# Optimization experiments

Hardware: AMD Instinct MI355X
Metric: run time of the kernel (lower is better)

The kernel has to match this reference:

```python
import jax, jax.numpy as jnp
import numpy as np


def setup_inputs() -> dict:
    key = jax.random.key(0)
    ks_ = jax.random.split(key, 12)
    B, Q, K, D, d = 8, 4096, 4096, 256, 64
    s = 1.0 / np.sqrt(D)
    inp = {
        "qs": jax.random.normal(ks_[0], (B, Q, D), jnp.float32),
        "ks": jax.random.normal(ks_[1], (B, K, D), jnp.float32),
        "vs": jax.random.normal(ks_[2], (B, K, D), jnp.float32),
        "valid_lens": jax.random.randint(ks_[3], (B,), 1, K + 1, jnp.int32),
        "Wq": jax.random.normal(ks_[4], (D, d), jnp.float32) * s,
        "bq": jnp.zeros((d,), jnp.float32),
        "Wk": jax.random.normal(ks_[5], (D, d), jnp.float32) * s,
        "bk": jnp.zeros((d,), jnp.float32),
        "Wv": jax.random.normal(ks_[6], (D, d), jnp.float32) * s,
        "bv": jnp.zeros((d,), jnp.float32),
        "Wo": jax.random.normal(ks_[7], (d, d), jnp.float32) * (1.0 / np.sqrt(d)),
        "bo": jnp.zeros((d,), jnp.float32),
    }
    return inp


def reference(qs, ks, vs, valid_lens, Wq, bq, Wk, bk, Wv, bv, Wo, bo):
    # Linear projections (default MLP([64]) heads)
    q = qs @ Wq + bq          # [B, Q, d]
    k = ks @ Wk + bk          # [B, K, d]
    v = vs @ Wv + bv          # [B, K, d]

    # RBF kernel scores: exp(-||q_i - k_j||^2 / sqrt(d)).
    # Expand ||q-k||^2 = ||q||^2 + ||k||^2 - 2 q.k to avoid the [B,Q,K,d]
    # pairwise-difference tensor the original materializes.
    q2 = jnp.sum(q * q, axis=-1)                         # [B, Q]
    k2 = jnp.sum(k * k, axis=-1)                         # [B, K]
    qk = jnp.einsum("bqd,bkd->bqk", q, k)                # [B, Q, K]
    d_sq = jnp.maximum(q2[:, :, None] + k2[:, None, :] - 2.0 * qk, 0.0)
    attn = jnp.exp(-d_sq / jnp.sqrt(jnp.asarray(k.shape[-1], q.dtype)))

    # Mask invalid keys (fill=0.0), then row-normalize.
    key_ids = jnp.arange(k.shape[1])                     # [K]
    mask = key_ids[None, None, :] < valid_lens[:, None, None]
    attn = jnp.where(mask, attn, 0.0)
    attn = attn / jnp.sum(attn, axis=-1, keepdims=True)

    ctx = attn @ v                                       # [B, Q, d]
    out = ctx @ Wo + bo                                  # [B, Q, d]
    return out, attn
```

## Files before the change

### kernel.cpp

```cpp
#include <hip/hip_runtime.h>
#include <hip/hip_bf16.h>


typedef _Float16 HALF;
typedef HALF half8 __attribute__((ext_vector_type(8)));
typedef float f32x4 __attribute__((ext_vector_type(4)));

#define MFMA16(a, b, c) __builtin_amdgcn_mfma_f32_16x16x32_f16((a), (b), (c), 0, 0, 0)

union Cv4 { HALF h[4]; uint2 u; };
union Cv8 { HALF h[8]; uint4 u; };

__global__ __launch_bounds__(256) void k_prep(const float* __restrict__ Wq,
                                              const float* __restrict__ Wk,
                                              const float* __restrict__ Wv,
                                              const float* __restrict__ Wo,
                                              HALF* __restrict__ wt,
                                              HALF* __restrict__ wto) {
    int gid = blockIdx.x * 256 + threadIdx.x;
    if (gid < 49152) {
        int t = gid >> 14;
        int rem = gid & 16383;
        int n = rem >> 8, k = rem & 255;
        const float* W = (t == 0) ? Wq : ((t == 1) ? Wk : Wv);
        wt[gid] = (HALF)W[k * 64 + n];
    } else {
        int rem = gid - 49152;
        int n = rem >> 6, k = rem & 63;
        wto[rem] = (HALF)Wo[k * 64 + n];
    }
}

__global__ __launch_bounds__(256) void k_proj(const float* __restrict__ qs,
                                              const float* __restrict__ ks,
                                              const float* __restrict__ vs,
                                              const float* __restrict__ bq,
                                              const float* __restrict__ bk,
                                              const float* __restrict__ bv,
                                              const HALF* __restrict__ wt,
                                              HALF* __restrict__ qh,
                                              HALF* __restrict__ kh,
                                              HALF* __restrict__ vth,
                                              float* __restrict__ q2w,
                                              float* __restrict__ k2w) {
    int bid = blockIdx.x;
    int t = bid >> 9;
    int rem = bid & 511;
    int b = rem & 7, rt = rem >> 3;
    int m0 = rt * 64;
    const float* X    = (t == 0) ? qs : ((t == 1) ? ks : vs);
    const float* bias = (t == 0) ? bq : ((t == 1) ? bk : bv);

    __shared__ char smem[67584];
    HALF (*sW)[264]  = (HALF(*)[264])smem;
    HALF (*sX)[264]  = (HALF(*)[264])(smem + 33792);
    float (*sOut)[68] = (float(*)[68])(smem + 33792);

    int tid = threadIdx.x;
    int w = tid >> 6, lane = tid & 63, ln = lane & 15, quad = lane >> 4;

    const HALF* wsrc = wt + t * 16384;
#pragma unroll
    for (int s = 0; s < 8; ++s) {
        int flat = (s * 256 + tid) * 8;
        int r = flat >> 8, c = flat & 255;
        *(uint4*)&sW[r][c] = *(const uint4*)(wsrc + flat);
    }
    const float* xbase = X + ((size_t)(b * 4096 + m0)) * 256;
#pragma unroll
    for (int s = 0; s < 16; ++s) {
        int flat = (s * 256 + tid) * 4;
        int r = flat >> 8, c = flat & 255;
        float4 xv = *(const float4*)(xbase + flat);
        Cv4 cv; cv.h[0] = (HALF)xv.x; cv.h[1] = (HALF)xv.y;
        cv.h[2] = (HALF)xv.z; cv.h[3] = (HALF)xv.w;
        *(uint2*)&sX[r][c] = cv.u;
    }
    __syncthreads();

    f32x4 zero4 = {0.f, 0.f, 0.f, 0.f};
    f32x4 acc[4] = {zero4, zero4, zero4, zero4};
#pragma unroll
    for (int kb = 0; kb < 8; ++kb) {
        half8 a = *(half8*)&sX[w * 16 + ln][kb * 32 + quad * 8];
#pragma unroll
        for (int t4 = 0; t4 < 4; ++t4) {
            half8 bf = *(half8*)&sW[t4 * 16 + ln][kb * 32 + quad * 8];
            acc[t4] = MFMA16(a, bf, acc[t4]);
        }
    }
    __syncthreads();

    float bias_v[4];
#pragma unroll
    for (int t4 = 0; t4 < 4; ++t4) bias_v[t4] = bias[t4 * 16 + ln];

    float rsq[4] = {0.f, 0.f, 0.f, 0.f};
#pragma unroll
    for (int t4 = 0; t4 < 4; ++t4) {
#pragma unroll
        for (int r = 0; r < 4; ++r) {
            float v = acc[t4][r] + bias_v[t4];
            rsq[r] += v * v;
            sOut[w * 16 + quad * 4 + r][t4 * 16 + ln] = v;
        }
    }
    if (t < 2) {
        float* dst2 = (t == 0) ? q2w : k2w;
#pragma unroll
        for (int r = 0; r < 4; ++r) {
            float v = rsq[r];
#pragma unroll
            for (int off = 1; off < 16; off <<= 1) v += __shfl_xor(v, off);
            if (ln == 0) dst2[b * 4096 + m0 + w * 16 + quad * 4 + r] = v;
        }
    }
    __syncthreads();

    if (t < 2) {
        HALF* dst = ((t == 0) ? qh : kh) + ((size_t)(b * 4096 + m0)) * 64;
#pragma unroll
        for (int s = 0; s < 4; ++s) {
            int flat = (s * 256 + tid) * 4;
            int r = flat >> 6, c = flat & 63;
            float4 v = *(float4*)&sOut[r][c];
            Cv4 cv; cv.h[0] = (HALF)v.x; cv.h[1] = (HALF)v.y;
            cv.h[2] = (HALF)v.z; cv.h[3] = (HALF)v.w;
            *(uint2*)(dst + flat) = cv.u;
        }
    } else {
        HALF* dst = vth + (size_t)b * 64 * 4096 + m0;
#pragma unroll
        for (int s = 0; s < 2; ++s) {
            int dv = s * 32 + (tid >> 3);
            int kc = (tid & 7) * 8;
            Cv8 cv;
#pragma unroll
            for (int i = 0; i < 8; ++i) cv.h[i] = (HALF)sOut[kc + i][dv];
            *(uint4*)(dst + (size_t)dv * 4096 + kc) = cv.u;
        }
    }
}

__global__ __launch_bounds__(256) void k_attn(const HALF* __restrict__ qh,
                                              const HALF* __restrict__ kh,
                                              const HALF* __restrict__ vth,
                                              const float* __restrict__ q2w,
                                              const float* __restrict__ k2w,
                                              const int* __restrict__ vlen,
                                              float* __restrict__ attn_out,
                                              float* __restrict__ ctx_out) {
    int bid = blockIdx.x;
    int b = bid & 7, qt = bid >> 3;
    int m0 = qt * 64;
    int tid = threadIdx.x;
    int w = tid >> 6, lane = tid & 63, ln = lane & 15, quad = lane >> 4;
    int valid = vlen[b];

    __shared__ char smem[36608];
    HALF (*sK)[72]  = (HALF(*)[72])smem;
    HALF (*sVt)[72] = (HALF(*)[72])(smem + 9216);
    float (*sS)[68] = (float(*)[68])(smem + 18432);
    HALF (*sQ)[72]  = (HALF(*)[72])(smem + 18432);
    float* sQ2 = (float*)(smem + 35840);
    float* sK2 = sQ2 + 64;
    float* sRS = sK2 + 64;

    const HALF* qbase = qh + ((size_t)(b * 4096 + m0)) * 64;
#pragma unroll
    for (int s = 0; s < 2; ++s) {
        int flat = (s * 256 + tid) * 8;
        *(uint4*)&sQ[flat >> 6][flat & 63] = *(const uint4*)(qbase + flat);
    }
    if (tid < 64) sQ2[tid] = q2w[b * 4096 + m0 + tid];
    __syncthreads();

    half8 qa[2];
    {
        int row = w * 16 + ln, k0 = quad * 8;
        qa[0] = *(half8*)&sQ[row][k0];
        qa[1] = *(half8*)&sQ[row][32 + k0];
    }
    __syncthreads();

    int nvt = (valid + 63) >> 6;
    const HALF* kbb = kh + (size_t)b * 4096 * 64;
    const HALF* vtb = vth + (size_t)b * 64 * 4096;

    float rs[4] = {0.f, 0.f, 0.f, 0.f};

    for (int nt = 0; nt < nvt; ++nt) {
        int n0 = nt * 64;
#pragma unroll
        for (int s = 0; s < 2; ++s) {
            int flat = (s * 256 + tid) * 8;
            *(uint4*)&sK[flat >> 6][flat & 63] = *(const uint4*)(kbb + (size_t)n0 * 64 + flat);
        }
        if (tid < 64) sK2[tid] = k2w[b * 4096 + n0 + tid];
        __syncthreads();
#pragma unroll
        for (int t4 = 0; t4 < 4; ++t4) {
            f32x4 acc = {0.f, 0.f, 0.f, 0.f};
            half8 b0 = *(half8*)&sK[t4 * 16 + ln][quad * 8];
            half8 b1 = *(half8*)&sK[t4 * 16 + ln][32 + quad * 8];
            acc = MFMA16(qa[0], b0, acc);
            acc = MFMA16(qa[1], b1, acc);
            int col = t4 * 16 + ln;
            float k2v = sK2[col];
            bool ok = (n0 + col) < valid;
#pragma unroll
            for (int r = 0; r < 4; ++r) {
                int row = w * 16 + quad * 4 + r;
                float dsq = fmaxf(sQ2[row] + k2v - 2.f * acc[r], 0.f);
                float e = ok ? __expf(-0.125f * dsq) : 0.f;
                rs[r] += e;
            }
        }
        __syncthreads();
    }

#pragma unroll
    for (int r = 0; r < 4; ++r) {
        float v = rs[r];
#pragma unroll
        for (int off = 1; off < 16; off <<= 1) v += __shfl_xor(v, off);
        rs[r] = v;
    }
    if (ln == 0) {
#pragma unroll
        for (int r = 0; r < 4; ++r) sRS[w * 16 + quad * 4 + r] = rs[r];
    }
    __syncthreads();
    if (tid < 64) sRS[tid] = 1.0f / sRS[tid];
    __syncthreads();
    float inv_r[4];
#pragma unroll
    for (int r = 0; r < 4; ++r) inv_r[r] = sRS[w * 16 + quad * 4 + r];

    f32x4 cz = {0.f, 0.f, 0.f, 0.f};
    f32x4 cacc[4] = {cz, cz, cz, cz};
    float* attn_base = attn_out + ((size_t)(b * 4096 + m0)) * 4096;

    for (int nt = 0; nt < nvt; ++nt) {
        int n0 = nt * 64;
#pragma unroll
        for (int s = 0; s < 2; ++s) {
            int flat = (s * 256 + tid) * 8;
            *(uint4*)&sK[flat >> 6][flat & 63] = *(const uint4*)(kbb + (size_t)n0 * 64 + flat);
        }
#pragma unroll
        for (int s = 0; s < 2; ++s) {
            int flat = (s * 256 + tid) * 8;
            int dv = flat >> 6, c = flat & 63;
            *(uint4*)&sVt[dv][c] = *(const uint4*)(vtb + (size_t)dv * 4096 + n0 + c);
        }
        if (tid < 64) sK2[tid] = k2w[b * 4096 + n0 + tid];
        __syncthreads();
#pragma unroll
        for (int t4 = 0; t4 < 4; ++t4) {
            f32x4 acc = {0.f, 0.f, 0.f, 0.f};
            half8 b0 = *(half8*)&sK[t4 * 16 + ln][quad * 8];
            half8 b1 = *(half8*)&sK[t4 * 16 + ln][32 + quad * 8];
            acc = MFMA16(qa[0], b0, acc);
            acc = MFMA16(qa[1], b1, acc);
            int col = t4 * 16 + ln;
            float k2v = sK2[col];
            bool ok = (n0 + col) < valid;
#pragma unroll
            for (int r = 0; r < 4; ++r) {
                int row = w * 16 + quad * 4 + r;
                float dsq = fmaxf(sQ2[row] + k2v - 2.f * acc[r], 0.f);
                float e = ok ? __expf(-0.125f * dsq) : 0.f;
                sS[row][col] = e * inv_r[r];
            }
        }
        __syncthreads();
#pragma unroll
        for (int s = 0; s < 4; ++s) {
            int row = s * 16 + (tid >> 4);
            int col = (tid & 15) * 4;
            *(float4*)(attn_base + (size_t)row * 4096 + n0 + col) = *(float4*)&sS[row][col];
        }
#pragma unroll
        for (int ks2 = 0; ks2 < 2; ++ks2) {
            int row_a = w * 16 + ln;
            const float* sp = &sS[row_a][ks2 * 32 + quad * 8];
            float4 f0 = *(float4*)sp;
            float4 f1 = *((float4*)sp + 1);
            half8 pa = {(HALF)f0.x, (HALF)f0.y, (HALF)f0.z, (HALF)f0.w,
                        (HALF)f1.x, (HALF)f1.y, (HALF)f1.z, (HALF)f1.w};
#pragma unroll
            for (int t4 = 0; t4 < 4; ++t4) {
                half8 vb = *(half8*)&sVt[t4 * 16 + ln][ks2 * 32 + quad * 8];
                cacc[t4] = MFMA16(pa, vb, cacc[t4]);
            }
        }
        __syncthreads();
    }

    float4 z4 = {0.f, 0.f, 0.f, 0.f};
    for (int nt = nvt; nt < 64; ++nt) {
        int n0 = nt * 64;
#pragma unroll
        for (int s = 0; s < 4; ++s) {
            int row = s * 16 + (tid >> 4);
            int col = (tid & 15) * 4;
            *(float4*)(attn_base + (size_t)row * 4096 + n0 + col) = z4;
        }
    }

    float* ctx_base = ctx_out + ((size_t)(b * 4096 + m0)) * 64;
#pragma unroll
    for (int t4 = 0; t4 < 4; ++t4) {
#pragma unroll
        for (int r = 0; r < 4; ++r) {
            ctx_base[(size_t)(w * 16 + quad * 4 + r) * 64 + t4 * 16 + ln] = cacc[t4][r];
        }
    }
}

__global__ __launch_bounds__(256) void k_out(float* __restrict__ outg,
                                             const HALF* __restrict__ wto,
                                             const float* __restrict__ bo) {
    int bid = blockIdx.x;
    size_t row0 = (size_t)bid * 64;
    int tid = threadIdx.x;
    int w = tid >> 6, lane = tid & 63, ln = lane & 15, quad = lane >> 4;

    __shared__ char smem[18432];
    HALF (*sA)[72] = (HALF(*)[72])smem;
    HALF (*sB)[72] = (HALF(*)[72])(smem + 9216);

    float* gbase = outg + row0 * 64;
#pragma unroll
    for (int s = 0; s < 4; ++s) {
        int flat = (s * 256 + tid) * 4;
        int r = flat >> 6, c = flat & 63;
        float4 v = *(const float4*)(gbase + flat);
        Cv4 cv; cv.h[0] = (HALF)v.x; cv.h[1] = (HALF)v.y;
        cv.h[2] = (HALF)v.z; cv.h[3] = (HALF)v.w;
        *(uint2*)&sA[r][c] = cv.u;
    }
#pragma unroll
    for (int s = 0; s < 2; ++s) {
        int flat = (s * 256 + tid) * 8;
        *(uint4*)&sB[flat >> 6][flat & 63] = *(const uint4*)(wto + flat);
    }
    __syncthreads();

    f32x4 z = {0.f, 0.f, 0.f, 0.f};
    f32x4 acc[4] = {z, z, z, z};
#pragma unroll
    for (int ks2 = 0; ks2 < 2; ++ks2) {
        half8 a = *(half8*)&sA[w * 16 + ln][ks2 * 32 + quad * 8];
#pragma unroll
        for (int t4 = 0; t4 < 4; ++t4) {
            half8 bf = *(half8*)&sB[t4 * 16 + ln][ks2 * 32 + quad * 8];
            acc[t4] = MFMA16(a, bf, acc[t4]);
        }
    }
#pragma unroll
    for (int t4 = 0; t4 < 4; ++t4) {
        float bov = bo[t4 * 16 + ln];
#pragma unroll
        for (int r = 0; r < 4; ++r) {
            gbase[(size_t)(w * 16 + quad * 4 + r) * 64 + t4 * 16 + ln] = acc[t4][r] + bov;
        }
    }
}

extern "C" void kernel_launch(void* const* d_in, const int* in_sizes, int n_in,
                              void* d_out, int out_size, void* d_ws, size_t ws_size,
                              hipStream_t stream) {
    const float* qs = (const float*)d_in[0];
    const float* ks = (const float*)d_in[1];
    const float* vs = (const float*)d_in[2];
    const int* vlen = (const int*)d_in[3];
    const float* Wq = (const float*)d_in[4];
    const float* bq = (const float*)d_in[5];
    const float* Wk = (const float*)d_in[6];
    const float* bk = (const float*)d_in[7];
    const float* Wv = (const float*)d_in[8];
    const float* bv = (const float*)d_in[9];
    const float* Wo = (const float*)d_in[10];
    const float* bo = (const float*)d_in[11];

    float* out  = (float*)d_out;
    float* attn = out + 2097152;

    char* wsb = (char*)d_ws;
    HALF*  wt  = (HALF*)(wsb + 0);
    HALF*  wto = (HALF*)(wsb + 98304);
    HALF*  qh  = (HALF*)(wsb + 131072);
    HALF*  kh  = (HALF*)(wsb + 4325376);
    HALF*  vth = (HALF*)(wsb + 8519680);
    float* q2w = (float*)(wsb + 12713984);
    float* k2w = (float*)(wsb + 12845056);

    k_prep<<<208, 256, 0, stream>>>(Wq, Wk, Wv, Wo, wt, wto);
    k_proj<<<1536, 256, 0, stream>>>(qs, ks, vs, bq, bk, bv, wt, qh, kh, vth, q2w, k2w);
    k_attn<<<512, 256, 0, stream>>>(qh, kh, vth, q2w, k2w, vlen, attn, out);
    k_out<<<512, 256, 0, stream>>>(out, wto, bo);
}
```

Measured before the change: 793.0 us.

## Drop query norm term, prefetch K/V tiles, fuse output projection into attention

Computes attention scores as exp(q·k/4 - |k|^2/8), dropping the per-row |q|^2 factor that cancels in normalization and folding the key mask into a -inf per-key constant. K/V tiles are prefetched into registers for the next iteration while the current tile is computed. The output projection kernel is fused into the attention epilogue, which avoids the ctx round-trip through global memory. Batch-to-block mapping is skewed for load balance, and packed fp16 conversion is used. Removing |q|^2 changes numerical scaling, so exp values can be much larger than before and may risk overflow for large dot products.

```diff
diff --git a/kernel.cpp b/kernel.cpp
--- a/kernel.cpp
+++ b/kernel.cpp
@@ -4,12 +4,14 @@
 
 typedef _Float16 HALF;
 typedef HALF half8 __attribute__((ext_vector_type(8)));
+typedef __fp16 fp16x2 __attribute__((ext_vector_type(2)));
 typedef float f32x4 __attribute__((ext_vector_type(4)));
 
 #define MFMA16(a, b, c) __builtin_amdgcn_mfma_f32_16x16x32_f16((a), (b), (c), 0, 0, 0)
 
 union Cv4 { HALF h[4]; uint2 u; };
 union Cv8 { HALF h[8]; uint4 u; };
+union PK8 { fp16x2 p2[4]; half8 v; };
 
 __global__ __launch_bounds__(256) void k_prep(const float* __restrict__ Wq,
                                               const float* __restrict__ Wk,
@@ -31,18 +33,17 @@
     }
 }
 
-__global__ __launch_bounds__(256) void k_proj(const float* __restrict__ qs,
-                                              const float* __restrict__ ks,
-                                              const float* __restrict__ vs,
-                                              const float* __restrict__ bq,
-                                              const float* __restrict__ bk,
-                                              const float* __restrict__ bv,
-                                              const HALF* __restrict__ wt,
-                                              HALF* __restrict__ qh,
-                                              HALF* __restrict__ kh,
-                                              HALF* __restrict__ vth,
-                                              float* __restrict__ q2w,
-                                              float* __restrict__ k2w) {
+__global__ __launch_bounds__(256, 2) void k_proj(const float* __restrict__ qs,
+                                                 const float* __restrict__ ks,
+                                                 const float* __restrict__ vs,
+                                                 const float* __restrict__ bq,
+                                                 const float* __restrict__ bk,
+                                                 const float* __restrict__ bv,
+                                                 const HALF* __restrict__ wt,
+                                                 HALF* __restrict__ qh,
+                                                 HALF* __restrict__ kh,
+                                                 HALF* __restrict__ vth,
+                                                 float* __restrict__ kcw) {
     int bid = blockIdx.x;
     int t = bid >> 9;
     int rem = bid & 511;
@@ -105,14 +106,13 @@
             sOut[w * 16 + quad * 4 + r][t4 * 16 + ln] = v;
         }
     }
-    if (t < 2) {
-        float* dst2 = (t == 0) ? q2w : k2w;
+    if (t == 1) {
 #pragma unroll
         for (int r = 0; r < 4; ++r) {
             float v = rsq[r];
 #pragma unroll
             for (int off = 1; off < 16; off <<= 1) v += __shfl_xor(v, off);
-            if (ln == 0) dst2[b * 4096 + m0 + w * 16 + quad * 4 + r] = v;
+            if (ln == 0) kcw[b * 4096 + m0 + w * 16 + quad * 4 + r] = -0.125f * v;
         }
     }
     __syncthreads();
@@ -142,79 +142,77 @@
     }
 }
 
-__global__ __launch_bounds__(256) void k_attn(const HALF* __restrict__ qh,
-                                              const HALF* __restrict__ kh,
-                                              const HALF* __restrict__ vth,
-                                              const float* __restrict__ q2w,
-                                              const float* __restrict__ k2w,
-                                              const int* __restrict__ vlen,
-                                              float* __restrict__ attn_out,
-                                              float* __restrict__ ctx_out) {
+__global__ __launch_bounds__(256, 4) void k_attn(const HALF* __restrict__ qh,
+                                                 const HALF* __restrict__ kh,
+                                                 const HALF* __restrict__ vth,
+                                                 const float* __restrict__ kcw,
+                                                 const int* __restrict__ vlen,
+                                                 const HALF* __restrict__ wto,
+                                                 const float* __restrict__ bo,
+                                                 float* __restrict__ attn_out,
+                                                 float* __restrict__ out) {
     int bid = blockIdx.x;
-    int b = bid & 7, qt = bid >> 3;
+    int qt = bid >> 3;
+    int b = (bid + qt) & 7;
     int m0 = qt * 64;
     int tid = threadIdx.x;
     int w = tid >> 6, lane = tid & 63, ln = lane & 15, quad = lane >> 4;
     int valid = vlen[b];
 
-    __shared__ char smem[36608];
+    __shared__ char smem[36352];
     HALF (*sK)[72]  = (HALF(*)[72])smem;
     HALF (*sVt)[72] = (HALF(*)[72])(smem + 9216);
     float (*sS)[68] = (float(*)[68])(smem + 18432);
     HALF (*sQ)[72]  = (HALF(*)[72])(smem + 18432);
-    float* sQ2 = (float*)(smem + 35840);
-    float* sK2 = sQ2 + 64;
-    float* sRS = sK2 + 64;
+    HALF (*sWo)[72] = (HALF(*)[72])smem;
+    float* sKC = (float*)(smem + 35840);
+    float* sRS = (float*)(smem + 36096);
 
     const HALF* qbase = qh + ((size_t)(b * 4096 + m0)) * 64;
-#pragma unroll
-    for (int s = 0; s < 2; ++s) {
-        int flat = (s * 256 + tid) * 8;
-        *(uint4*)&sQ[flat >> 6][flat & 63] = *(const uint4*)(qbase + flat);
-    }
-    if (tid < 64) sQ2[tid] = q2w[b * 4096 + m0 + tid];
-    __syncthreads();
-
-    half8 qa[2];
-    {
-        int row = w * 16 + ln, k0 = quad * 8;
-        qa[0] = *(half8*)&sQ[row][k0];
-        qa[1] = *(half8*)&sQ[row][32 + k0];
-    }
+    { int f0 = tid * 8;         *(uint4*)&sQ[f0 >> 6][f0 & 63] = *(const uint4*)(qbase + f0);
+      int f1 = (256 + tid) * 8; *(uint4*)&sQ[f1 >> 6][f1 & 63] = *(const uint4*)(qbase + f1); }
+    __syncthreads();
+    half8 qa0, qa1;
+    { int row = w * 16 + ln, k0 = quad * 8;
+      qa0 = *(half8*)&sQ[row][k0];
+      qa1 = *(half8*)&sQ[row][32 + k0]; }
     __syncthreads();
 
     int nvt = (valid + 63) >> 6;
     const HALF* kbb = kh + (size_t)b * 4096 * 64;
     const HALF* vtb = vth + (size_t)b * 64 * 4096;
+    const float* kcb = kcw + b * 4096;
+    const float NEG_INF = -__builtin_inff();
+
+    uint4 kr0, kr1; float kcr = 0.f;
+    kr0 = *(const uint4*)(kbb + tid * 8);
+    kr1 = *(const uint4*)(kbb + (256 + tid) * 8);
+    if (tid < 64) kcr = kcb[tid];
 
     float rs[4] = {0.f, 0.f, 0.f, 0.f};
-
     for (int nt = 0; nt < nvt; ++nt) {
         int n0 = nt * 64;
-#pragma unroll
-        for (int s = 0; s < 2; ++s) {
-            int flat = (s * 256 + tid) * 8;
-            *(uint4*)&sK[flat >> 6][flat & 63] = *(const uint4*)(kbb + (size_t)n0 * 64 + flat);
-        }
-        if (tid < 64) sK2[tid] = k2w[b * 4096 + n0 + tid];
-        __syncthreads();
+        { int f0 = tid * 8;         *(uint4*)&sK[f0 >> 6][f0 & 63] = kr0;
+          int f1 = (256 + tid) * 8; *(uint4*)&sK[f1 >> 6][f1 & 63] = kr1; }
+        if (tid < 64) sKC[tid] = (n0 + tid < valid) ? kcr : NEG_INF;
+        __syncthreads();
+        if (nt + 1 < nvt) {
+            const HALF* src = kbb + (size_t)(nt + 1) * 4096;
+            kr0 = *(const uint4*)(src + tid * 8);
+            kr1 = *(const uint4*)(src + (256 + tid) * 8);
+            if (tid < 64) kcr = kcb[n0 + 64 + tid];
+        }
 #pragma unroll
         for (int t4 = 0; t4 < 4; ++t4) {
             f32x4 acc = {0.f, 0.f, 0.f, 0.f};
             half8 b0 = *(half8*)&sK[t4 * 16 + ln][quad * 8];
             half8 b1 = *(half8*)&sK[t4 * 16 + ln][32 + quad * 8];
-            acc = MFMA16(qa[0], b0, acc);
-            acc = MFMA16(qa[1], b1, acc);
-            int col = t4 * 16 + ln;
-            float k2v = sK2[col];
-            bool ok = (n0 + col) < valid;
-#pragma unroll
-            for (int r = 0; r < 4; ++r) {
-                int row = w * 16 + quad * 4 + r;
-                float dsq = fmaxf(sQ2[row] + k2v - 2.f * acc[r], 0.f);
-                float e = ok ? __expf(-0.125f * dsq) : 0.f;
-                rs[r] += e;
-            }
+            acc = MFMA16(qa0, b0, acc);
+            acc = MFMA16(qa1, b1, acc);
+            float kcv = sKC[t4 * 16 + ln];
+#pragma unroll
+            for (int r = 0; r < 4; ++r)
+                rs[r] += __expf(fmaf(acc[r], 0.25f, kcv));
         }
         __syncthreads();
     }
@@ -241,37 +239,45 @@
     f32x4 cacc[4] = {cz, cz, cz, cz};
     float* attn_base = attn_out + ((size_t)(b * 4096 + m0)) * 4096;
 
+    uint4 vr0, vr1;
+    kr0 = *(const uint4*)(kbb + tid * 8);
+    kr1 = *(const uint4*)(kbb + (256 + tid) * 8);
+    { int f0 = tid * 8, f1 = (256 + tid) * 8;
+      vr0 = *(const uint4*)(vtb + (size_t)(f0 >> 6) * 4096 + (f0 & 63));
+      vr1 = *(const uint4*)(vtb + (size_t)(f1 >> 6) * 4096 + (f1 & 63)); }
+    if (tid < 64) kcr = kcb[tid];
+
     for (int nt = 0; nt < nvt; ++nt) {
         int n0 = nt * 64;
-#pragma unroll
-        for (int s = 0; s < 2; ++s) {
-            int flat = (s * 256 + tid) * 8;
-            *(uint4*)&sK[flat >> 6][flat & 63] = *(const uint4*)(kbb + (size_t)n0 * 64 + flat);
-        }
-#pragma unroll
-        for (int s = 0; s < 2; ++s) {
-            int flat = (s * 256 + tid) * 8;
-            int dv = flat >> 6, c = flat & 63;
-            *(uint4*)&sVt[dv][c] = *(const uint4*)(vtb + (size_t)dv * 4096 + n0 + c);
-        }
-        if (tid < 64) sK2[tid] = k2w[b * 4096 + n0 + tid];
-        __syncthreads();
+        { int f0 = tid * 8, f1 = (256 + tid) * 8;
+          *(uint4*)&sK[f0 >> 6][f0 & 63] = kr0;
+          *(uint4*)&sK[f1 >> 6][f1 & 63] = kr1;
+          *(uint4*)&sVt[f0 >> 6][f0 & 63] = vr0;
+          *(uint4*)&sVt[f1 >> 6][f1 & 63] = vr1; }
+        if (tid < 64) sKC[tid] = (n0 + tid < valid) ? kcr : NEG_INF;
+        __syncthreads();
+        if (nt + 1 < nvt) {
+            const HALF* ksrc = kbb + (size_t)(nt + 1) * 4096;
+            int f0 = tid * 8, f1 = (256 + tid) * 8;
+            kr0 = *(const uint4*)(ksrc + f0);
+            kr1 = *(const uint4*)(ksrc + f1);
+            vr0 = *(const uint4*)(vtb + (size_t)(f0 >> 6) * 4096 + n0 + 64 + (f0 & 63));
+            vr1 = *(const uint4*)(vtb + (size_t)(f1 >> 6) * 4096 + n0 + 64 + (f1 & 63));
+            if (tid < 64) kcr = kcb[n0 + 64 + tid];
+        }
 #pragma unroll
         for (int t4 = 0; t4 < 4; ++t4) {
             f32x4 acc = {0.f, 0.f, 0.f, 0.f};
             half8 b0 = *(half8*)&sK[t4 * 16 + ln][quad * 8];
             half8 b1 = *(half8*)&sK[t4 * 16 + ln][32 + quad * 8];
-            acc = MFMA16(qa[0], b0, acc);
-            acc = MFMA16(qa[1], b1, acc);
+            acc = MFMA16(qa0, b0, acc);
+            acc = MFMA16(qa1, b1, acc);
             int col = t4 * 16 + ln;
-            float k2v = sK2[col];
-            bool ok = (n0 + col) < valid;
+            float kcv = sKC[col];
 #pragma unroll
             for (int r = 0; r < 4; ++r) {
                 int row = w * 16 + quad * 4 + r;
-                float dsq = fmaxf(sQ2[row] + k2v - 2.f * acc[r], 0.f);
-                float e = ok ? __expf(-0.125f * dsq) : 0.f;
-                sS[row][col] = e * inv_r[r];
+                sS[row][col] = __expf(fmaf(acc[r], 0.25f, kcv)) * inv_r[r];
             }
         }
         __syncthreads();
@@ -283,12 +289,15 @@
         }
 #pragma unroll
         for (int ks2 = 0; ks2 < 2; ++ks2) {
-            int row_a = w * 16 + ln;
-            const float* sp = &sS[row_a][ks2 * 32 + quad * 8];
+            const float* sp = &sS[w * 16 + ln][ks2 * 32 + quad * 8];
             float4 f0 = *(float4*)sp;
             float4 f1 = *((float4*)sp + 1);
-            half8 pa = {(HALF)f0.x, (HALF)f0.y, (HALF)f0.z, (HALF)f0.w,
-                        (HALF)f1.x, (HALF)f1.y, (HALF)f1.z, (HALF)f1.w};
+            PK8 pk;
+            pk.p2[0] = __builtin_amdgcn_cvt_pkrtz(f0.x, f0.y);
+            pk.p2[1] = __builtin_amdgcn_cvt_pkrtz(f0.z, f0.w);
+            pk.p2[2] = __builtin_amdgcn_cvt_pkrtz(f1.x, f1.y);
+            pk.p2[3] = __builtin_amdgcn_cvt_pkrtz(f1.z, f1.w);
+            half8 pa = pk.v;
 #pragma unroll
             for (int t4 = 0; t4 < 4; ++t4) {
                 half8 vb = *(half8*)&sVt[t4 * 16 + ln][ks2 * 32 + quad * 8];
@@ -309,63 +318,41 @@
         }
     }
 
-    float* ctx_base = ctx_out + ((size_t)(b * 4096 + m0)) * 64;
 #pragma unroll
     for (int t4 = 0; t4 < 4; ++t4) {
 #pragma unroll
-        for (int r = 0; r < 4; ++r) {
-            ctx_base[(size_t)(w * 16 + quad * 4 + r) * 64 + t4 * 16 + ln] = cacc[t4][r];
-        }
-    }
-}
-
-__global__ __launch_bounds__(256) void k_out(float* __restrict__ outg,
-                                             const HALF* __restrict__ wto,
-                                             const float* __restrict__ bo) {
-    int bid = blockIdx.x;
-    size_t row0 = (size_t)bid * 64;
-    int tid = threadIdx.x;
-    int w = tid >> 6, lane = tid & 63, ln = lane & 15, quad = lane >> 4;
-
-    __shared__ char smem[18432];
-    HALF (*sA)[72] = (HALF(*)[72])smem;
-    HALF (*sB)[72] = (HALF(*)[72])(smem + 9216);
-
-    float* gbase = outg + row0 * 64;
-#pragma unroll
-    for (int s = 0; s < 4; ++s) {
-        int flat = (s * 256 + tid) * 4;
-        int r = flat >> 6, c = flat & 63;
-        float4 v = *(const float4*)(gbase + flat);
-        Cv4 cv; cv.h[0] = (HALF)v.x; cv.h[1] = (HALF)v.y;
-        cv.h[2] = (HALF)v.z; cv.h[3] = (HALF)v.w;
-        *(uint2*)&sA[r][c] = cv.u;
-    }
-#pragma unroll
-    for (int s = 0; s < 2; ++s) {
-        int flat = (s * 256 + tid) * 8;
-        *(uint4*)&sB[flat >> 6][flat & 63] = *(const uint4*)(wto + flat);
-    }
-    __syncthreads();
-
-    f32x4 z = {0.f, 0.f, 0.f, 0.f};
-    f32x4 acc[4] = {z, z, z, z};
+        for (int r = 0; r < 4; ++r)
+            sS[w * 16 + quad * 4 + r][t4 * 16 + ln] = cacc[t4][r];
+    }
+    { int f0 = tid * 8;         *(uint4*)&sWo[f0 >> 6][f0 & 63] = *(const uint4*)(wto + f0);
+      int f1 = (256 + tid) * 8; *(uint4*)&sWo[f1 >> 6][f1 & 63] = *(const uint4*)(wto + f1); }
+    __syncthreads();
+
+    f32x4 oacc[4] = {cz, cz, cz, cz};
 #pragma unroll
     for (int ks2 = 0; ks2 < 2; ++ks2) {
-        half8 a = *(half8*)&sA[w * 16 + ln][ks2 * 32 + quad * 8];
+        const float* sp = &sS[w * 16 + ln][ks2 * 32 + quad * 8];
+        float4 f0 = *(float4*)sp;
+        float4 f1 = *((float4*)sp + 1);
+        PK8 pk;
+        pk.p2[0] = __builtin_amdgcn_cvt_pkrtz(f0.x, f0.y);
+        pk.p2[1] = __builtin_amdgcn_cvt_pkrtz(f0.z, f0.w);
+        pk.p2[2] = __builtin_amdgcn_cvt_pkrtz(f1.x, f1.y);
+        pk.p2[3] = __builtin_amdgcn_cvt_pkrtz(f1.z, f1.w);
+        half8 a = pk.v;
 #pragma unroll
         for (int t4 = 0; t4 < 4; ++t4) {
-            half8 bf = *(half8*)&sB[t4 * 16 + ln][ks2 * 32 + quad * 8];
-            acc[t4] = MFMA16(a, bf, acc[t4]);
-        }
-    }
+            half8 bf = *(half8*)&sWo[t4 * 16 + ln][ks2 * 32 + quad * 8];
+            oacc[t4] = MFMA16(a, bf, oacc[t4]);
+        }
+    }
+    float* obase = out + ((size_t)(b * 4096 + m0)) * 64;
 #pragma unroll
     for (int t4 = 0; t4 < 4; ++t4) {
         float bov = bo[t4 * 16 + ln];
 #pragma unroll
-        for (int r = 0; r < 4; ++r) {
-            gbase[(size_t)(w * 16 + quad * 4 + r) * 64 + t4 * 16 + ln] = acc[t4][r] + bov;
-        }
+        for (int r = 0; r < 4; ++r)
+            obase[(size_t)(w * 16 + quad * 4 + r) * 64 + t4 * 16 + ln] = oacc[t4][r] + bov;
     }
 }
 
@@ -394,11 +381,9 @@
     HALF*  qh  = (HALF*)(wsb + 131072);
     HALF*  kh  = (HALF*)(wsb + 4325376);
     HALF*  vth = (HALF*)(wsb + 8519680);
-    float* q2w = (float*)(wsb + 12713984);
-    float* k2w = (float*)(wsb + 12845056);
+    float* kcw = (float*)(wsb + 12713984);
 
     k_prep<<<208, 256, 0, stream>>>(Wq, Wk, Wv, Wo, wt, wto);
-    k_proj<<<1536, 256, 0, stream>>>(qs, ks, vs, bq, bk, bv, wt, qh, kh, vth, q2w, k2w);
-    k_attn<<<512, 256, 0, stream>>>(qh, kh, vth, q2w, k2w, vlen, attn, out);
-    k_out<<<512, 256, 0, stream>>>(out, wto, bo);
+    k_proj<<<1536, 256, 0, stream>>>(qs, ks, vs, bq, bk, bv, wt, qh, kh, vth, kcw);
+    k_attn<<<512, 256, 0, stream>>>(qh, kh, vth, kcw, vlen, wto, bo, attn, out);
 }
```

New measurement: 688.1 us. 1.15x faster.
